# Kernel tuning notes

Hardware: AMD Instinct MI355X
Metric: run time of the kernel (lower is better)

## Reference

```python
import jax, jax.numpy as jnp
import numpy as np

EMBED_DIM = 1024
SEQ = 1024  # must equal EMBED_DIM due to the module's mask construction
BATCH = 8


def setup_inputs() -> dict:
    key = jax.random.key(0)
    ks = jax.random.split(key, 7)
    s = 1.0 / np.sqrt(EMBED_DIM)
    return {
        "x": jax.random.normal(ks[0], (BATCH, SEQ, EMBED_DIM), jnp.float32),
        "Wq": jax.random.normal(ks[1], (EMBED_DIM, EMBED_DIM), jnp.float32) * s,
        "bq": jax.random.normal(ks[2], (EMBED_DIM,), jnp.float32) * s,
        "Wk": jax.random.normal(ks[3], (EMBED_DIM, EMBED_DIM), jnp.float32) * s,
        "bk": jax.random.normal(ks[4], (EMBED_DIM,), jnp.float32) * s,
        "Wv": jax.random.normal(ks[5], (EMBED_DIM, EMBED_DIM), jnp.float32) * s,
        "bv": jax.random.normal(ks[6], (EMBED_DIM,), jnp.float32) * s,
    }


def reference(x, Wq, bq, Wk, bk, Wv, bv):
    # nn.Linear: y = x @ W.T + b
    q = jnp.einsum("bse,oe->bso", x, Wq) + bq
    k = jnp.einsum("bse,oe->bso", x, Wk) + bk
    v = jnp.einsum("bse,oe->bso", x, Wv) + bv
    scores = jnp.einsum("bqd,bkd->bqk", q, k) / jnp.sqrt(jnp.float32(EMBED_DIM))
    # causal mask: tril(ones(E, E)) applied to [B, S, S] scores (S == E)
    causal = jnp.tril(jnp.ones((SEQ, SEQ), dtype=bool))
    scores = jnp.where(causal, scores, jnp.float32(-1e9))
    attn = jax.nn.softmax(scores, axis=-1)
    return jnp.einsum("bqk,bkd->bqd", attn, v)
```

## Files before the change

kernel.cpp:

```cpp
#include <hip/hip_runtime.h>
#include <hip/hip_bf16.h>

typedef unsigned short u16;
typedef __bf16 bf16x8 __attribute__((ext_vector_type(8)));
typedef float f32x4 __attribute__((ext_vector_type(4)));

#define AS1 __attribute__((address_space(1)))
#define AS3 __attribute__((address_space(3)))

__device__ inline void gload_lds16(const void* g, void* l) {
    __builtin_amdgcn_global_load_lds((const AS1 void*)g, (AS3 void*)l, 16, 0, 0);
}

__device__ inline u16 f2bf(float f) {
    __hip_bfloat16 h = __float2bfloat16(f);
    return __builtin_bit_cast(u16, h);
}
__device__ inline float bf2f(unsigned u) {
    return __builtin_bit_cast(float, u << 16);
}

__global__ __launch_bounds__(256)
void cvt_all(const float4* __restrict__ x,  const float4* __restrict__ wq,
             const float4* __restrict__ wk, const float4* __restrict__ wv,
             u16* __restrict__ xb, u16* __restrict__ Wb) {
    int i = blockIdx.x * 256 + threadIdx.x;
    const float4* src; u16* dst; int off;
    if (i < 2097152)      { src = x;  dst = xb;            off = i; }
    else if (i < 2359296) { src = wq; dst = Wb;            off = i - 2097152; }
    else if (i < 2621440) { src = wk; dst = Wb + 1048576;  off = i - 2359296; }
    else                  { src = wv; dst = Wb + 2097152;  off = i - 2621440; }
    float4 v = src[off];
    uint2 pk;
    pk.x = (unsigned)f2bf(v.x) | ((unsigned)f2bf(v.y) << 16);
    pk.y = (unsigned)f2bf(v.z) | ((unsigned)f2bf(v.w) << 16);
    *(uint2*)(dst + (long long)off * 4) = pk;
}

__global__ __launch_bounds__(256)
void proj_qkv(const u16* __restrict__ xb, const u16* __restrict__ Wb,
              u16* __restrict__ QK, u16* __restrict__ Vt,
              const float* __restrict__ bq, const float* __restrict__ bk)
{
    constexpr int BK = 64, K = 1024;
    __shared__ __align__(16) u16 shA[128 * BK];
    __shared__ __align__(16) u16 shB[128 * BK];
    const int z = blockIdx.z;
    int row0, col0;
    const u16 *Ab, *Bb;
    if (z < 2) {
        row0 = (blockIdx.x * 8 + (blockIdx.y & 7)) * 128;
        col0 = (int)(blockIdx.y >> 3) * 128;
        Ab = xb + (long long)row0 * K;
        Bb = Wb + (long long)z * 1048576 + (long long)col0 * K;
    } else {
        col0 = (blockIdx.x * 8 + (blockIdx.y & 7)) * 128;
        row0 = (int)(blockIdx.y >> 3) * 128;
        Ab = Wb + 2097152 + (long long)row0 * K;
        Bb = xb + (long long)col0 * K;
    }
    u16* Cb = (z < 2) ? (QK + (long long)z * 8388608) : Vt;
    const int ldC = (z < 2) ? 1024 : 8192;
    const float* bp = (z == 1) ? bk : bq;

    const int t  = (int)threadIdx.x;
    const int l  = t & 63;
    const int w  = t >> 6;
    const int wr = w >> 1, wc = w & 1;
    const int fr = l & 15, fq = l >> 4;

    f32x4 acc[4][4];
    #pragma unroll
    for (int m = 0; m < 4; ++m)
        #pragma unroll
        for (int n = 0; n < 4; ++n)
            acc[m][n] = (f32x4){0.f, 0.f, 0.f, 0.f};

    int aOff[2][4], bOff[2][4];
    #pragma unroll
    for (int kh = 0; kh < 2; ++kh) {
        const int g = ((kh * 4 + fq) ^ (fr & 7)) * 8;
        #pragma unroll
        for (int m = 0; m < 4; ++m) aOff[kh][m] = (wr * 64 + m * 16 + fr) * 64 + g;
        #pragma unroll
        for (int n = 0; n < 4; ++n) bOff[kh][n] = (wc * 64 + n * 16 + fr) * 64 + g;
    }

    for (int kk = 0; kk < K; kk += BK) {
        if (kk) __syncthreads();
        #pragma unroll
        for (int r = 0; r < 4; ++r) {
            const int s  = t + r * 256;
            const int rw = s >> 3;
            const int g  = (s & 7) ^ (rw & 7);
            gload_lds16(Ab + (long long)rw * K + kk + g * 8, (void*)(shA + s * 8));
            gload_lds16(Bb + (long long)rw * K + kk + g * 8, (void*)(shB + s * 8));
        }
        __syncthreads();
        bf16x8 aF[2][4], bF[2][4];
        #pragma unroll
        for (int kh = 0; kh < 2; ++kh) {
            #pragma unroll
            for (int m = 0; m < 4; ++m) aF[kh][m] = *(const bf16x8*)(shA + aOff[kh][m]);
            #pragma unroll
            for (int n = 0; n < 4; ++n) bF[kh][n] = *(const bf16x8*)(shB + bOff[kh][n]);
        }
        #pragma unroll
        for (int kh = 0; kh < 2; ++kh)
            #pragma unroll
            for (int m = 0; m < 4; ++m)
                #pragma unroll
                for (int n = 0; n < 4; ++n)
                    acc[m][n] = __builtin_amdgcn_mfma_f32_16x16x32_bf16(aF[kh][m], bF[kh][n], acc[m][n], 0, 0, 0);
    }

    #pragma unroll
    for (int n = 0; n < 4; ++n) {
        const int cn = col0 + wc * 64 + n * 16 + fr;
        const float cb = (z < 2) ? bp[cn] : 0.0f;
        #pragma unroll
        for (int m = 0; m < 4; ++m) {
            const int cm = row0 + wr * 64 + m * 16 + fq * 4;
            #pragma unroll
            for (int j = 0; j < 4; ++j)
                Cb[(long long)(cm + j) * ldC + cn] = f2bf(acc[m][n][j] + cb);
        }
    }
}

template<int MODE>
__global__ __launch_bounds__(256)
void gemm_bt(const u16* __restrict__ A, long long strideAb,
             const u16* __restrict__ Bt, long long strideBb,
             void* __restrict__ Cv, long long strideCb,
             const float* __restrict__ bias,
             int K, int strideBrow, float scale)
{
    constexpr int BK = 64;
    __shared__ __align__(16) u16 shA[128 * BK];
    __shared__ __align__(16) u16 shB[128 * BK];
    int bz, row0, col0;
    if (MODE == 1) {
        bz   = blockIdx.x;
        row0 = blockIdx.y * 128;
        col0 = blockIdx.z * 128;
    } else {
        bz   = blockIdx.x;
        row0 = (7 - (int)blockIdx.y) * 128;
        col0 = blockIdx.z * 128;
    }
    if (MODE == 1 && col0 > row0) return;
    const u16* Ab = A  + bz * strideAb + (long long)row0 * K;
    const u16* Bb = Bt + bz * strideBb + (long long)col0 * strideBrow;
    int kEnd = K;
    if (MODE == 2) kEnd = row0 + 128;

    const int t  = (int)threadIdx.x;
    const int l  = t & 63;
    const int w  = t >> 6;
    const int wr = w >> 1, wc = w & 1;
    const int fr = l & 15, fq = l >> 4;

    f32x4 acc[4][4];
    #pragma unroll
    for (int m = 0; m < 4; ++m)
        #pragma unroll
        for (int n = 0; n < 4; ++n)
            acc[m][n] = (f32x4){0.f, 0.f, 0.f, 0.f};

    int aOff[2][4], bOff[2][4];
    #pragma unroll
    for (int kh = 0; kh < 2; ++kh) {
        const int g = ((kh * 4 + fq) ^ (fr & 7)) * 8;
        #pragma unroll
        for (int m = 0; m < 4; ++m) aOff[kh][m] = (wr * 64 + m * 16 + fr) * 64 + g;
        #pragma unroll
        for (int n = 0; n < 4; ++n) bOff[kh][n] = (wc * 64 + n * 16 + fr) * 64 + g;
    }

    for (int kk = 0; kk < kEnd; kk += BK) {
        if (kk) __syncthreads();
        #pragma unroll
        for (int r = 0; r < 4; ++r) {
            const int s  = t + r * 256;
            const int rw = s >> 3;
            const int g  = (s & 7) ^ (rw & 7);
            gload_lds16(Ab + (long long)rw * K + kk + g * 8, (void*)(shA + s * 8));
            gload_lds16(Bb + (long long)rw * strideBrow + kk + g * 8, (void*)(shB + s * 8));
        }
        __syncthreads();
        bf16x8 aF[2][4], bF[2][4];
        #pragma unroll
        for (int kh = 0; kh < 2; ++kh) {
            #pragma unroll
            for (int m = 0; m < 4; ++m) aF[kh][m] = *(const bf16x8*)(shA + aOff[kh][m]);
            #pragma unroll
            for (int n = 0; n < 4; ++n) bF[kh][n] = *(const bf16x8*)(shB + bOff[kh][n]);
        }
        #pragma unroll
        for (int kh = 0; kh < 2; ++kh)
            #pragma unroll
            for (int m = 0; m < 4; ++m)
                #pragma unroll
                for (int n = 0; n < 4; ++n)
                    acc[m][n] = __builtin_amdgcn_mfma_f32_16x16x32_bf16(aF[kh][m], bF[kh][n], acc[m][n], 0, 0, 0);
    }

    if (MODE == 1) {
        u16* C = (u16*)Cv + bz * strideCb;
        #pragma unroll
        for (int n = 0; n < 4; ++n) {
            const int cn = col0 + wc * 64 + n * 16 + fr;
            #pragma unroll
            for (int m = 0; m < 4; ++m) {
                const int cm = row0 + wr * 64 + m * 16 + fq * 4;
                #pragma unroll
                for (int j = 0; j < 4; ++j)
                    C[(long long)(cm + j) * 1024 + cn] = f2bf(acc[m][n][j] * scale);
            }
        }
    } else {
        float* C = (float*)Cv + bz * strideCb;
        #pragma unroll
        for (int n = 0; n < 4; ++n) {
            const int cn = col0 + wc * 64 + n * 16 + fr;
            const float bvv = bias[cn];
            #pragma unroll
            for (int m = 0; m < 4; ++m) {
                const int cm = row0 + wr * 64 + m * 16 + fq * 4;
                #pragma unroll
                for (int j = 0; j < 4; ++j)
                    C[(long long)(cm + j) * 1024 + cn] = acc[m][n][j] + bvv;
            }
        }
    }
}

__global__ __launch_bounds__(256)
void softmax_causal(const u16* __restrict__ S, u16* __restrict__ P) {
    __shared__ float redM[4], redS[4];
    const int row = blockIdx.x;
    const int q   = row & 1023;
    const int t   = (int)threadIdx.x;
    const int l   = t & 63, w = t >> 6;
    const int j0  = t * 4;
    float x0 = -1e30f, x1 = -1e30f, x2 = -1e30f, x3 = -1e30f;
    if (j0 <= q) {
        uint2 raw = *(const uint2*)(S + (long long)row * 1024 + j0);
        x0 = bf2f(raw.x & 0xffffu);
        x1 = (j0 + 1 <= q) ? bf2f(raw.x >> 16) : -1e30f;
        x2 = (j0 + 2 <= q) ? bf2f(raw.y & 0xffffu) : -1e30f;
        x3 = (j0 + 3 <= q) ? bf2f(raw.y >> 16) : -1e30f;
    }
    float m = fmaxf(fmaxf(x0, x1), fmaxf(x2, x3));
    #pragma unroll
    for (int o = 32; o > 0; o >>= 1) m = fmaxf(m, __shfl_xor(m, o, 64));
    if (l == 0) redM[w] = m;
    __syncthreads();
    m = fmaxf(fmaxf(redM[0], redM[1]), fmaxf(redM[2], redM[3]));
    float e0 = __expf(x0 - m);
    float e1 = __expf(x1 - m);
    float e2 = __expf(x2 - m);
    float e3 = __expf(x3 - m);
    float s = e0 + e1 + e2 + e3;
    #pragma unroll
    for (int o = 32; o > 0; o >>= 1) s += __shfl_xor(s, o, 64);
    if (l == 0) redS[w] = s;
    __syncthreads();
    s = redS[0] + redS[1] + redS[2] + redS[3];
    const float inv = 1.0f / s;
    const int jmax = ((q >> 7) + 1) << 7;
    if (j0 < jmax) {
        uint2 pk;
        pk.x = (unsigned)f2bf(e0 * inv) | ((unsigned)f2bf(e1 * inv) << 16);
        pk.y = (unsigned)f2bf(e2 * inv) | ((unsigned)f2bf(e3 * inv) << 16);
        *(uint2*)(P + (long long)row * 1024 + j0) = pk;
    }
}

extern "C" void kernel_launch(void* const* d_in, const int* in_sizes, int n_in,
                              void* d_out, int out_size, void* d_ws, size_t ws_size,
                              hipStream_t stream) {
    const float* x  = (const float*)d_in[0];
    const float* Wq = (const float*)d_in[1];
    const float* bq = (const float*)d_in[2];
    const float* Wk = (const float*)d_in[3];
    const float* bk = (const float*)d_in[4];
    const float* Wv = (const float*)d_in[5];
    const float* bv = (const float*)d_in[6];
    float* out = (float*)d_out;
    char* ws = (char*)d_ws;

    u16* xb  = (u16*)(ws + 0);
    u16* Wb  = (u16*)(ws + ((size_t)16 << 20));
    u16* QK  = (u16*)(ws + ((size_t)22 << 20));
    u16* Vt  = (u16*)(ws + ((size_t)54 << 20));
    u16* SC  = (u16*)(ws + ((size_t)70 << 20));
    u16* P   = (u16*)(ws + ((size_t)86 << 20));

    cvt_all<<<11264, 256, 0, stream>>>((const float4*)x, (const float4*)Wq,
                                       (const float4*)Wk, (const float4*)Wv, xb, Wb);

    proj_qkv<<<dim3(8, 64, 3), 256, 0, stream>>>(xb, Wb, QK, Vt, bq, bk);

    gemm_bt<1><<<dim3(8, 8, 8), 256, 0, stream>>>(QK, 1048576LL, QK + 8388608LL, 1048576LL,
                                                  SC, 1048576LL, nullptr,
                                                  1024, 1024, 0.03125f);

    softmax_causal<<<8192, 256, 0, stream>>>(SC, P);

    gemm_bt<2><<<dim3(8, 8, 8), 256, 0, stream>>>(P, 1048576LL, Vt, 1024LL, out, 1048576LL,
                                                  bv, 1024, 8192, 1.0f);
}
```

Baseline: 114.0 us.

## Split QK projection into 256x256 double-buffered 8-wave kernel with phased MFMA schedule

The Q and K projections move from the shared 128x128 proj_qkv kernel into a new 512-thread kernel with 256x256 tiles. It double-buffers LDS via global_load_lds, interleaves LDS fragment reads with four MFMA phases separated by barriers, and raises priority around the MFMA phases with s_setprio. The V projection becomes its own 128x128 kernel. Larger tiles cut global traffic per FLOP and the pipeline aims to hide load latency, at the cost of 128KB of LDS per block, fewer blocks (256) and an extra kernel launch.

```diff
diff --git a/kernel.cpp b/kernel.cpp
--- a/kernel.cpp
+++ b/kernel.cpp
@@ -7,6 +7,7 @@
 
 #define AS1 __attribute__((address_space(1)))
 #define AS3 __attribute__((address_space(3)))
+#define MEMFENCE asm volatile("" ::: "memory")
 
 __device__ inline void gload_lds16(const void* g, void* l) {
     __builtin_amdgcn_global_load_lds((const AS1 void*)g, (AS3 void*)l, 16, 0, 0);
@@ -37,31 +38,191 @@
     *(uint2*)(dst + (long long)off * 4) = pk;
 }
 
+__global__ __launch_bounds__(512)
+void proj_qk8(const u16* __restrict__ xb, const u16* __restrict__ Wb,
+              u16* __restrict__ QK,
+              const float* __restrict__ bq, const float* __restrict__ bk)
+{
+    constexpr int K = 1024;
+    __shared__ __align__(16) u16 shA[2][256 * 64];
+    __shared__ __align__(16) u16 shB[2][256 * 64];
+    const int z    = blockIdx.z;
+    const int row0 = (blockIdx.x * 4 + (blockIdx.y & 3)) * 256;
+    const int col0 = (int)(blockIdx.y >> 2) * 256;
+    const u16* Ab = xb + (long long)row0 * K;
+    const u16* Bb = Wb + (long long)z * 1048576 + (long long)col0 * K;
+
+    const int t = (int)threadIdx.x, l = t & 63, w = t >> 6;
+    const int wr = w >> 2, wc = w & 3;
+    const int fr = l & 15, fq = l >> 4;
+
+    int sgel[4];
+    #pragma unroll
+    for (int r = 0; r < 4; ++r) {
+        const int s  = r * 512 + t;
+        const int rw = s >> 3;
+        const int g  = (s & 7) ^ (rw & 7);
+        sgel[r] = rw * K + g * 8;
+    }
+
+    const int g0  = fq ^ (fr & 7);
+    const int g1  = (4 + fq) ^ (fr & 7);
+    const int aB0 = (wr * 128 + fr) * 64 + g0 * 8;
+    const int aB1 = (wr * 128 + fr) * 64 + g1 * 8;
+    const int bB0 = (wc * 64 + fr) * 64 + g0 * 8;
+    const int bB1 = (wc * 64 + fr) * 64 + g1 * 8;
+
+    f32x4 acc[8][4];
+    #pragma unroll
+    for (int m = 0; m < 8; ++m)
+        #pragma unroll
+        for (int n = 0; n < 4; ++n) acc[m][n] = (f32x4){0.f, 0.f, 0.f, 0.f};
+
+    #pragma unroll
+    for (int r = 0; r < 4; ++r) {
+        const int s8 = (r * 512 + t) * 8;
+        gload_lds16(Ab + sgel[r], (u16*)shA[0] + s8);
+        gload_lds16(Bb + sgel[r], (u16*)shB[0] + s8);
+    }
+    asm volatile("s_waitcnt vmcnt(0)" ::: "memory");
+    __builtin_amdgcn_s_barrier();
+    MEMFENCE;
+
+    for (int kt = 0; kt < 16; ++kt) {
+        const u16* bA = shA[kt & 1];
+        const u16* bB = shB[kt & 1];
+        u16* nA = (u16*)shA[(kt + 1) & 1];
+        u16* nB = (u16*)shB[(kt + 1) & 1];
+        const int ko = (kt + 1) * 64;
+        const bool st = (kt < 15);
+        bf16x8 aF[2][4], bFa[2][2], bFb[2][2];
+
+        #pragma unroll
+        for (int mm = 0; mm < 4; ++mm) {
+            aF[0][mm] = *(const bf16x8*)(bA + aB0 + mm * 1024);
+            aF[1][mm] = *(const bf16x8*)(bA + aB1 + mm * 1024);
+        }
+        #pragma unroll
+        for (int n = 0; n < 2; ++n) {
+            bFa[0][n] = *(const bf16x8*)(bB + bB0 + n * 1024);
+            bFa[1][n] = *(const bf16x8*)(bB + bB1 + n * 1024);
+        }
+        if (st) {
+            #pragma unroll
+            for (int r = 0; r < 4; ++r) {
+                const int s8 = (r * 512 + t) * 8;
+                gload_lds16(Ab + sgel[r] + ko, nA + s8);
+                gload_lds16(Bb + sgel[r] + ko, nB + s8);
+            }
+        }
+        MEMFENCE;
+        __builtin_amdgcn_s_barrier();
+        asm volatile("s_waitcnt lgkmcnt(0)" ::: "memory");
+        __builtin_amdgcn_sched_barrier(0);
+        __builtin_amdgcn_s_setprio(1);
+        #pragma unroll
+        for (int mm = 0; mm < 4; ++mm)
+            #pragma unroll
+            for (int n = 0; n < 2; ++n) {
+                acc[mm][n] = __builtin_amdgcn_mfma_f32_16x16x32_bf16(aF[0][mm], bFa[0][n], acc[mm][n], 0, 0, 0);
+                acc[mm][n] = __builtin_amdgcn_mfma_f32_16x16x32_bf16(aF[1][mm], bFa[1][n], acc[mm][n], 0, 0, 0);
+            }
+        __builtin_amdgcn_s_setprio(0);
+        MEMFENCE;
+        __builtin_amdgcn_s_barrier();
+
+        #pragma unroll
+        for (int n = 0; n < 2; ++n) {
+            bFb[0][n] = *(const bf16x8*)(bB + bB0 + (2 + n) * 1024);
+            bFb[1][n] = *(const bf16x8*)(bB + bB1 + (2 + n) * 1024);
+        }
+        MEMFENCE;
+        __builtin_amdgcn_s_barrier();
+        asm volatile("s_waitcnt lgkmcnt(0)" ::: "memory");
+        __builtin_amdgcn_sched_barrier(0);
+        __builtin_amdgcn_s_setprio(1);
+        #pragma unroll
+        for (int mm = 0; mm < 4; ++mm)
+            #pragma unroll
+            for (int n = 0; n < 2; ++n) {
+                acc[mm][2 + n] = __builtin_amdgcn_mfma_f32_16x16x32_bf16(aF[0][mm], bFb[0][n], acc[mm][2 + n], 0, 0, 0);
+                acc[mm][2 + n] = __builtin_amdgcn_mfma_f32_16x16x32_bf16(aF[1][mm], bFb[1][n], acc[mm][2 + n], 0, 0, 0);
+            }
+        __builtin_amdgcn_s_setprio(0);
+        MEMFENCE;
+        __builtin_amdgcn_s_barrier();
+
+        #pragma unroll
+        for (int mm = 0; mm < 4; ++mm) {
+            aF[0][mm] = *(const bf16x8*)(bA + aB0 + 4096 + mm * 1024);
+            aF[1][mm] = *(const bf16x8*)(bA + aB1 + 4096 + mm * 1024);
+        }
+        MEMFENCE;
+        __builtin_amdgcn_s_barrier();
+        asm volatile("s_waitcnt lgkmcnt(0)" ::: "memory");
+        __builtin_amdgcn_sched_barrier(0);
+        __builtin_amdgcn_s_setprio(1);
+        #pragma unroll
+        for (int mm = 0; mm < 4; ++mm)
+            #pragma unroll
+            for (int n = 0; n < 2; ++n) {
+                acc[4 + mm][2 + n] = __builtin_amdgcn_mfma_f32_16x16x32_bf16(aF[0][mm], bFb[0][n], acc[4 + mm][2 + n], 0, 0, 0);
+                acc[4 + mm][2 + n] = __builtin_amdgcn_mfma_f32_16x16x32_bf16(aF[1][mm], bFb[1][n], acc[4 + mm][2 + n], 0, 0, 0);
+            }
+        __builtin_amdgcn_s_setprio(0);
+        MEMFENCE;
+        __builtin_amdgcn_s_barrier();
+
+        #pragma unroll
+        for (int n = 0; n < 2; ++n) {
+            bFa[0][n] = *(const bf16x8*)(bB + bB0 + n * 1024);
+            bFa[1][n] = *(const bf16x8*)(bB + bB1 + n * 1024);
+        }
+        MEMFENCE;
+        __builtin_amdgcn_s_barrier();
+        asm volatile("s_waitcnt lgkmcnt(0)" ::: "memory");
+        __builtin_amdgcn_sched_barrier(0);
+        __builtin_amdgcn_s_setprio(1);
+        #pragma unroll
+        for (int mm = 0; mm < 4; ++mm)
+            #pragma unroll
+            for (int n = 0; n < 2; ++n) {
+                acc[4 + mm][n] = __builtin_amdgcn_mfma_f32_16x16x32_bf16(aF[0][mm], bFa[0][n], acc[4 + mm][n], 0, 0, 0);
+                acc[4 + mm][n] = __builtin_amdgcn_mfma_f32_16x16x32_bf16(aF[1][mm], bFa[1][n], acc[4 + mm][n], 0, 0, 0);
+            }
+        __builtin_amdgcn_s_setprio(0);
+        asm volatile("s_waitcnt vmcnt(0)" ::: "memory");
+        MEMFENCE;
+        __builtin_amdgcn_s_barrier();
+    }
+
+    const float* bp = z ? bk : bq;
+    u16* C = QK + (long long)z * 8388608;
+    #pragma unroll
+    for (int n = 0; n < 4; ++n) {
+        const int cn = col0 + wc * 64 + n * 16 + fr;
+        const float cb = bp[cn];
+        #pragma unroll
+        for (int m = 0; m < 8; ++m) {
+            const int cm = row0 + wr * 128 + m * 16 + fq * 4;
+            #pragma unroll
+            for (int j = 0; j < 4; ++j)
+                C[(long long)(cm + j) * 1024 + cn] = f2bf(acc[m][n][j] + cb);
+        }
+    }
+}
+
 __global__ __launch_bounds__(256)
-void proj_qkv(const u16* __restrict__ xb, const u16* __restrict__ Wb,
-              u16* __restrict__ QK, u16* __restrict__ Vt,
-              const float* __restrict__ bq, const float* __restrict__ bk)
+void proj_v(const u16* __restrict__ Wv, const u16* __restrict__ xb,
+            u16* __restrict__ Vt)
 {
     constexpr int BK = 64, K = 1024;
     __shared__ __align__(16) u16 shA[128 * BK];
     __shared__ __align__(16) u16 shB[128 * BK];
-    const int z = blockIdx.z;
-    int row0, col0;
-    const u16 *Ab, *Bb;
-    if (z < 2) {
-        row0 = (blockIdx.x * 8 + (blockIdx.y & 7)) * 128;
-        col0 = (int)(blockIdx.y >> 3) * 128;
-        Ab = xb + (long long)row0 * K;
-        Bb = Wb + (long long)z * 1048576 + (long long)col0 * K;
-    } else {
-        col0 = (blockIdx.x * 8 + (blockIdx.y & 7)) * 128;
-        row0 = (int)(blockIdx.y >> 3) * 128;
-        Ab = Wb + 2097152 + (long long)row0 * K;
-        Bb = xb + (long long)col0 * K;
-    }
-    u16* Cb = (z < 2) ? (QK + (long long)z * 8388608) : Vt;
-    const int ldC = (z < 2) ? 1024 : 8192;
-    const float* bp = (z == 1) ? bk : bq;
+    const int col0 = (blockIdx.x * 8 + (blockIdx.y & 7)) * 128;
+    const int row0 = (int)(blockIdx.y >> 3) * 128;
+    const u16* Ab = Wv + (long long)row0 * K;
+    const u16* Bb = xb + (long long)col0 * K;
 
     const int t  = (int)threadIdx.x;
     const int l  = t & 63;
@@ -117,13 +278,12 @@
     #pragma unroll
     for (int n = 0; n < 4; ++n) {
         const int cn = col0 + wc * 64 + n * 16 + fr;
-        const float cb = (z < 2) ? bp[cn] : 0.0f;
         #pragma unroll
         for (int m = 0; m < 4; ++m) {
             const int cm = row0 + wr * 64 + m * 16 + fq * 4;
             #pragma unroll
             for (int j = 0; j < 4; ++j)
-                Cb[(long long)(cm + j) * ldC + cn] = f2bf(acc[m][n][j] + cb);
+                Vt[(long long)(cm + j) * 8192 + cn] = f2bf(acc[m][n][j]);
         }
     }
 }
@@ -301,7 +461,9 @@
     cvt_all<<<11264, 256, 0, stream>>>((const float4*)x, (const float4*)Wq,
                                        (const float4*)Wk, (const float4*)Wv, xb, Wb);
 
-    proj_qkv<<<dim3(8, 64, 3), 256, 0, stream>>>(xb, Wb, QK, Vt, bq, bk);
+    proj_qk8<<<dim3(8, 16, 2), 512, 0, stream>>>(xb, Wb, QK, bq, bk);
+
+    proj_v<<<dim3(8, 64), 256, 0, stream>>>(Wb + 2097152, xb, Vt);
 
     gemm_bt<1><<<dim3(8, 8, 8), 256, 0, stream>>>(QK, 1048576LL, QK + 8388608LL, 1048576LL,
                                                   SC, 1048576LL, nullptr,
```

New measurement: 125.4 us. 1.1x slower.
